# Optimization experiments

Measured on AMD Instinct MI355X. Metric: run time of the kernel, lower is better.

## Reference

```python
import jax, jax.numpy as jnp
import numpy as np

D_IN, D_OUT, K = 128, 256, 16
B, N = 2, 16384
D_HALF = D_OUT // 2
EPS = 1e-6
GROUPS = 16


def conv1x1(x, w, b):
    # x: (B,C,N,K), w: (O,C), b: (O,)
    return jnp.einsum('oc,bcnk->bonk', w, x) + b[None, :, None, None]


def groupnorm(x, w, b, groups=GROUPS):
    Bv, C, Nv, Kv = x.shape
    xr = x.reshape(Bv, groups, C // groups, Nv, Kv)
    m = xr.mean(axis=(2, 3, 4), keepdims=True)
    v = xr.var(axis=(2, 3, 4), keepdims=True)
    xn = ((xr - m) / jnp.sqrt(v + EPS)).reshape(Bv, C, Nv, Kv)
    return xn * w[None, :, None, None] + b[None, :, None, None]


def lse(coords, x, idx, dist, w, b, gw, gb):
    # coords: (B,N,3); x: (B,C,N,1); idx: (B,N,K); dist: (B,N,K)
    nbr = jax.vmap(lambda c, i: c[i])(coords, idx)          # (B,N,K,3)
    ctr = jnp.broadcast_to(coords[:, :, None, :], nbr.shape)  # (B,N,K,3)
    rel = jnp.concatenate([ctr, nbr, ctr - nbr], axis=-1)    # (B,N,K,9)
    geo = jnp.concatenate([rel.transpose(0, 3, 1, 2), dist[:, None, :, :]], axis=1)  # (B,10,N,K)
    geo = jax.nn.relu(groupnorm(conv1x1(geo, w, b), gw, gb))  # (B,d/2,N,K)
    nf = jax.vmap(lambda f, i: f[:, i])(x[..., 0], idx)       # (B,d/2,N,K)
    return jnp.concatenate([geo, nf], axis=1)                 # (B,d,N,K)


def attentive_pool(x, w, b, gw, gb):
    m = x.mean(axis=-1, keepdims=True)  # (B,C,N,1)
    return jax.nn.relu(groupnorm(conv1x1(m, w, b), gw, gb))


def setup_inputs() -> dict:
    key = jax.random.key(0)
    ks = jax.random.split(key, 16)
    s = 0.02
    d = {
        'coords': jax.random.normal(ks[0], (B, N, 3), jnp.float32),
        'features': jax.random.normal(ks[1], (B, D_IN, N, 1), jnp.float32),
        'knn_dist': jax.random.uniform(ks[2], (B, N, K), jnp.float32),
        'knn_idx': jax.random.randint(ks[3], (B, N, K), 0, N),
        'w1': jax.random.normal(ks[4], (D_HALF, D_IN), jnp.float32) * s,
        'b1': jnp.zeros((D_HALF,), jnp.float32),
        'lse1_w': jax.random.normal(ks[5], (D_HALF, 10), jnp.float32) * s,
        'lse1_b': jnp.zeros((D_HALF,), jnp.float32),
        'lse1_gw': jnp.ones((D_HALF,), jnp.float32),
        'lse1_gb': jnp.zeros((D_HALF,), jnp.float32),
        'pool1_w': jax.random.normal(ks[6], (D_HALF, D_OUT), jnp.float32) * s,
        'pool1_b': jnp.zeros((D_HALF,), jnp.float32),
        'pool1_gw': jnp.ones((D_HALF,), jnp.float32),
        'pool1_gb': jnp.zeros((D_HALF,), jnp.float32),
        'lse2_w': jax.random.normal(ks[7], (D_HALF, 10), jnp.float32) * s,
        'lse2_b': jnp.zeros((D_HALF,), jnp.float32),
        'lse2_gw': jnp.ones((D_HALF,), jnp.float32),
        'lse2_gb': jnp.zeros((D_HALF,), jnp.float32),
        'pool2_w': jax.random.normal(ks[8], (D_OUT, D_OUT), jnp.float32) * s,
        'pool2_b': jnp.zeros((D_OUT,), jnp.float32),
        'pool2_gw': jnp.ones((D_OUT,), jnp.float32),
        'pool2_gb': jnp.zeros((D_OUT,), jnp.float32),
        'mlp2_w': jax.random.normal(ks[9], (2 * D_OUT, D_OUT), jnp.float32) * s,
        'mlp2_b': jnp.zeros((2 * D_OUT,), jnp.float32),
        'sc_w': jax.random.normal(ks[10], (2 * D_OUT, D_IN), jnp.float32) * s,
        'sc_b': jnp.zeros((2 * D_OUT,), jnp.float32),
        'sc_gw': jnp.ones((2 * D_OUT,), jnp.float32),
        'sc_gb': jnp.zeros((2 * D_OUT,), jnp.float32),
    }
    return d


def reference(coords, features, knn_dist, knn_idx,
              w1, b1,
              lse1_w, lse1_b, lse1_gw, lse1_gb,
              pool1_w, pool1_b, pool1_gw, pool1_gb,
              lse2_w, lse2_b, lse2_gw, lse2_gb,
              pool2_w, pool2_b, pool2_gw, pool2_gb,
              mlp2_w, mlp2_b, sc_w, sc_b, sc_gw, sc_gb):
    # mlp1: conv + LeakyReLU(0.2), no norm
    x = jax.nn.leaky_relu(conv1x1(features, w1, b1), 0.2)        # (B,d/2,N,1)
    x = lse(coords, x, knn_idx, knn_dist, lse1_w, lse1_b, lse1_gw, lse1_gb)  # (B,d,N,K)
    x = attentive_pool(x, pool1_w, pool1_b, pool1_gw, pool1_gb)  # (B,d/2,N,1)
    x = lse(coords, x, knn_idx, knn_dist, lse2_w, lse2_b, lse2_gw, lse2_gb)  # (B,d,N,K)
    x = attentive_pool(x, pool2_w, pool2_b, pool2_gw, pool2_gb)  # (B,d,N,1)
    main = conv1x1(x, mlp2_w, mlp2_b)                            # (B,2d,N,1)
    short = groupnorm(conv1x1(features, sc_w, sc_b), sc_gw, sc_gb)
    return jax.nn.leaky_relu(main + short, 0.01)                 # (B,2d,N,1)
```

## Files before the change

kernel.cpp:

```cpp
#include <hip/hip_runtime.h>


constexpr int Bc = 2;
constexpr int Nc = 16384;
constexpr int Kc = 16;
constexpr float EPSc = 1e-6f;

typedef __attribute__((ext_vector_type(8))) short short8;
typedef __attribute__((ext_vector_type(4))) short short4v;
typedef __attribute__((ext_vector_type(4))) float floatx4;

__device__ inline short f2bf(float x) {
    union { float f; unsigned u; } v; v.f = x;
    unsigned r = v.u + 0x7fffu + ((v.u >> 16) & 1u);
    return (short)(r >> 16);
}
__device__ inline float bf2f(short s) {
    union { unsigned u; float f; } v;
    v.u = ((unsigned)(unsigned short)s) << 16;
    return v.f;
}

constexpr size_t OW_P1W = 0;
constexpr size_t OW_P2W = OW_P1W + 128*256;
constexpr size_t OW_M2W = OW_P2W + 256*256;
constexpr size_t OW_SCW = OW_M2W + 512*256;
constexpr size_t OW_W1  = OW_SCW + 512*128;
constexpr size_t OW_L1W = OW_W1  + 128*128;
constexpr size_t OW_L2W = OW_L1W + 128*32;
constexpr size_t OW_FB  = OW_L2W + 128*32;
constexpr size_t OW_X1  = OW_FB  + (size_t)Bc*Nc*128;
constexpr size_t OW_M   = OW_X1  + (size_t)Bc*Nc*128;
constexpr size_t OW_Z1  = OW_M   + (size_t)Bc*Nc*256;
constexpr size_t OW_Z2  = OW_Z1  + (size_t)Bc*Nc*128;
constexpr size_t OW_S   = OW_Z2  + (size_t)Bc*Nc*256;

constexpr int CV0 = 128*256;
constexpr int CV1 = CV0 + 256*256;
constexpr int CV2 = CV1 + 512*256;
constexpr int CV3 = CV2 + 512*128;
constexpr int CV4 = CV3 + 128*128;
constexpr int CV5 = CV4 + 128*32;
constexpr int CV6 = CV5 + 128*32;
constexpr int CVTOT = CV6 + 512;

__global__ void prep_kernel(const float* __restrict__ p1w,
                            const float* __restrict__ p2w,
                            const float* __restrict__ m2w,
                            const float* __restrict__ scw,
                            const float* __restrict__ w1,
                            const float* __restrict__ l1w,
                            const float* __restrict__ l2w,
                            short* __restrict__ W16,
                            float* __restrict__ ST)
{
    int i = blockIdx.x * 256 + threadIdx.x;
    if (i < CV0) { W16[OW_P1W + i] = f2bf(p1w[i]); return; }
    if (i < CV1) { int k = i - CV0; W16[OW_P2W + k] = f2bf(p2w[k]); return; }
    if (i < CV2) { int k = i - CV1; W16[OW_M2W + k] = f2bf(m2w[k]); return; }
    if (i < CV3) { int k = i - CV2; W16[OW_SCW + k] = f2bf(scw[k]); return; }
    if (i < CV4) { int k = i - CV3; W16[OW_W1  + k] = f2bf(w1[k]); return; }
    if (i < CV5) { int k = i - CV4; int o = k >> 5, c = k & 31;
                   W16[OW_L1W + k] = (c < 10) ? f2bf(l1w[o*10+c]) : (short)0; return; }
    if (i < CV6) { int k = i - CV5; int o = k >> 5, c = k & 31;
                   W16[OW_L2W + k] = (c < 10) ? f2bf(l2w[o*10+c]) : (short)0; return; }
    { int k = i - CV6; if (k < 512) ST[k] = 0.f; }
}

__global__ void feat_t_kernel(const float* __restrict__ in, short* __restrict__ out) {
    int tid  = threadIdx.x;
    int lane = tid & 63, wave = tid >> 6;
    int bb = blockIdx.x / (Nc / 64);
    int n  = (blockIdx.x % (Nc / 64)) * 64 + lane;
    #pragma unroll
    for (int cc = 0; cc < 4; cc++) {
        int c0 = (wave + cc * 4) * 8;
        short8 sv;
        #pragma unroll
        for (int i = 0; i < 8; i++)
            sv[i] = f2bf(in[((size_t)bb * 128 + c0 + i) * Nc + n]);
        *(short8*)&out[((size_t)(bb * Nc + n)) * 128 + c0] = sv;
    }
}

__launch_bounds__(256)
__global__ void geo_reduce_kernel(const float* __restrict__ coords,
                                  const int* __restrict__ knn_idx,
                                  const float* __restrict__ knn_dist,
                                  float* __restrict__ dst)
{
    __shared__ float part[4][65];
    const int tid  = threadIdx.x;
    const int b    = blockIdx.y;
    const int base = blockIdx.x * 256 + tid;
    const float* cb  = coords   + (size_t)b * Nc * 3;
    const int*   ib  = knn_idx  + (size_t)b * Nc * Kc;
    const float* db  = knn_dist + (size_t)b * Nc * Kc;

    float acc[65];
    #pragma unroll
    for (int i = 0; i < 65; i++) acc[i] = 0.f;

    #pragma unroll
    for (int it = 0; it < 4; it++) {
        int r = base + it * 65536;
        int n = r >> 4;
        float cx = cb[n*3+0], cy = cb[n*3+1], cz = cb[n*3+2];
        int   j  = ib[r];
        float nx = cb[j*3+0], ny = cb[j*3+1], nz = cb[j*3+2];
        float d  = db[r];
        float g[10] = {cx,cy,cz,nx,ny,nz,cx-nx,cy-ny,cz-nz,d};
        #pragma unroll
        for (int c = 0; c < 10; c++) acc[c] += g[c];
        int idx = 10;
        #pragma unroll
        for (int c = 0; c < 10; c++)
            #pragma unroll
            for (int c2 = c; c2 < 10; c2++) acc[idx++] += g[c] * g[c2];
    }
    #pragma unroll
    for (int i = 0; i < 65; i++) {
        float v = acc[i];
        #pragma unroll
        for (int off = 1; off < 64; off <<= 1) v += __shfl_xor(v, off);
        acc[i] = v;
    }
    int lane = tid & 63, wave = tid >> 6;
    if (lane == 0) {
        #pragma unroll
        for (int i = 0; i < 65; i++) part[wave][i] = acc[i];
    }
    __syncthreads();
    if (tid < 65) {
        float s = part[0][tid] + part[1][tid] + part[2][tid] + part[3][tid];
        atomicAdd(&dst[b * 65 + tid], s);
    }
}

__launch_bounds__(512)
__global__ void lse_param_kernel(const float* __restrict__ geoS,
                                 const float* __restrict__ l1w,
                                 const float* __restrict__ l1b,
                                 const float* __restrict__ l1gw,
                                 const float* __restrict__ l1gb,
                                 const float* __restrict__ l2w,
                                 const float* __restrict__ l2b,
                                 const float* __restrict__ l2gw,
                                 const float* __restrict__ l2gb,
                                 float* __restrict__ lp)
{
    __shared__ float osum[512], osq[512];
    const int tid = threadIdx.x;
    const int s = tid >> 8, r = tid & 255, b = r >> 7, o = r & 127;
    const float* wf = s ? l2w : l1w;
    const float* bf = s ? l2b : l1b;
    const float* gwf = s ? l2gw : l1gw;
    const float* gbf = s ? l2gb : l1gb;
    const float NK = (float)(Nc * Kc);
    const float* S = geoS + b * 65;

    float w[10];
    #pragma unroll
    for (int c = 0; c < 10; c++) w[c] = wf[o * 10 + c];
    float wS = 0.f;
    #pragma unroll
    for (int c = 0; c < 10; c++) wS += w[c] * S[c];
    float q = 0.f;
    {
        int idx = 10;
        #pragma unroll
        for (int c = 0; c < 10; c++)
            #pragma unroll
            for (int c2 = c; c2 < 10; c2++) {
                float t = w[c] * w[c2] * S[idx++];
                q += (c == c2) ? t : 2.f * t;
            }
    }
    float bo = bf[o];
    osum[tid] = NK * bo + wS;
    osq[tid]  = NK * bo * bo + 2.f * bo * wS + q;
    __syncthreads();
    int gb0 = tid & ~7;
    float gs = 0.f, gq = 0.f;
    #pragma unroll
    for (int i = 0; i < 8; i++) { gs += osum[gb0 + i]; gq += osq[gb0 + i]; }
    float cnt  = 8.f * NK;
    float mean = gs / cnt;
    float var  = gq / cnt - mean * mean;
    float iv   = rsqrtf(var + EPSc);
    float psc  = iv * gwf[o];
    float psh  = (bo - mean) * psc + gbf[o];
    lp[s * 512 + b * 256 + o]       = psc;
    lp[s * 512 + b * 256 + 128 + o] = psh;
}

template<int CIN, int COUT, int GROUP_CH, int MODE>
__launch_bounds__(256)
__global__ void gemm_conv(const short* __restrict__ wA,
                          const short* __restrict__ xB,
                          const float* __restrict__ bias,
                          short* __restrict__ outb,
                          float* __restrict__ outf,
                          float* __restrict__ stats,
                          const short* __restrict__ sbuf,
                          const float* __restrict__ st_sc,
                          const float* __restrict__ gw,
                          const float* __restrict__ gb,
                          float sc_cnt,
                          const float* __restrict__ bst,
                          const float* __restrict__ bgw,
                          const float* __restrict__ bgb,
                          float bcnt,
                          const float* __restrict__ bias2,
                          short* __restrict__ outb2)
{
    __shared__ short Abuf[128 * 40];
    __shared__ short Bbuf[128 * 40];
    __shared__ float sstat[32];
    __shared__ float smean[4], sinv[4];
    __shared__ float bsc[256], bsh[256];

    const int tid  = threadIdx.x;
    const int n0   = blockIdx.x * 128;
    const int mo   = blockIdx.y * 128;
    const int b    = blockIdx.z;
    const int lane = tid & 63;
    const int wave = tid >> 6;
    const int wm   = (wave >> 1) * 64;
    const int wn   = (wave & 1) * 64;
    const int l15  = lane & 15;
    const int quad = lane >> 4;
    const bool sc_tile = (MODE == 4) && (mo < 512);

    if constexpr (MODE == 2 || MODE == 4) { if (tid < 32) sstat[tid] = 0.f; }
    if constexpr (MODE == 3) {
        if (tid < 4) {
            int g = (mo >> 5) + tid;
            float s0 = st_sc[(b * 16 + g) * 2 + 0];
            float s1 = st_sc[(b * 16 + g) * 2 + 1];
            float mean = s0 / sc_cnt;
            float var  = s1 / sc_cnt - mean * mean;
            smean[tid] = mean;
            sinv[tid]  = rsqrtf(var + EPSc);
        }
        if (tid < CIN) {
            int g = tid >> 4;
            float s0 = bst[(b * 16 + g) * 2 + 0];
            float s1 = bst[(b * 16 + g) * 2 + 1];
            float mean = s0 / bcnt;
            float var  = s1 / bcnt - mean * mean;
            float inv  = rsqrtf(var + EPSc);
            float sc_  = inv * bgw[tid];
            bsc[tid] = sc_;
            bsh[tid] = bgb[tid] - mean * sc_;
        }
    }

    floatx4 acc[4][4];
    #pragma unroll
    for (int mi = 0; mi < 4; mi++)
        #pragma unroll
        for (int ni = 0; ni < 4; ni++)
            acc[mi][ni] = (floatx4){0.f, 0.f, 0.f, 0.f};

    const short* wAr = wA + (size_t)mo * CIN;
    const short* xBr = xB + (size_t)b * Nc * CIN + (size_t)n0 * CIN;

    for (int c0 = 0; c0 < CIN; c0 += 32) {
        __syncthreads();
        #pragma unroll
        for (int s = 0; s < 2; s++) {
            int e = tid + s * 256;
            int r = e >> 2, q = e & 3;
            *(short8*)&Abuf[r * 40 + q * 8] =
                *(const short8*)(wAr + (size_t)r * CIN + c0 + q * 8);
            short8 v = *(const short8*)(xBr + (size_t)r * CIN + c0 + q * 8);
            if constexpr (MODE == 3) {
                #pragma unroll
                for (int i = 0; i < 8; i++) {
                    int ch = c0 + q * 8 + i;
                    float t = bf2f(v[i]) * bsc[ch] + bsh[ch];
                    v[i] = f2bf(t > 0.f ? t : 0.f);
                }
            }
            *(short8*)&Bbuf[r * 40 + q * 8] = v;
        }
        __syncthreads();

        short8 af[4], bfr[4];
        #pragma unroll
        for (int mi = 0; mi < 4; mi++)
            af[mi] = *(short8*)&Abuf[(wm + mi * 16 + l15) * 40 + quad * 8];
        #pragma unroll
        for (int ni = 0; ni < 4; ni++)
            bfr[ni] = *(short8*)&Bbuf[(wn + ni * 16 + l15) * 40 + quad * 8];
        #pragma unroll
        for (int mi = 0; mi < 4; mi++)
            #pragma unroll
            for (int ni = 0; ni < 4; ni++)
                acc[mi][ni] = __builtin_amdgcn_mfma_f32_16x16x32_bf16(
                    af[mi], bfr[ni], acc[mi][ni], 0, 0, 0);
    }

    #pragma unroll
    for (int mi = 0; mi < 4; mi++) {
        int rowl = wm + mi * 16 + quad * 4;
        float b4[4], gw4[4], gb4[4];
        #pragma unroll
        for (int r = 0; r < 4; r++) {
            if constexpr (MODE == 4) {
                b4[r] = sc_tile ? bias[mo + rowl + r] : bias2[mo - 512 + rowl + r];
            } else {
                b4[r] = bias[mo + rowl + r];
            }
            if constexpr (MODE == 3) {
                gw4[r] = gw[mo + rowl + r];
                gb4[r] = gb[mo + rowl + r];
            }
        }
        float gs = 0.f, gq = 0.f;
        #pragma unroll
        for (int ni = 0; ni < 4; ni++) {
            int col = n0 + wn + ni * 16 + l15;
            if constexpr (MODE == 3) {
                short4v s4 = *(const short4v*)&sbuf[((size_t)(b * Nc + col)) * 512 + mo + rowl];
                int gl = rowl >> 5;
                #pragma unroll
                for (int r = 0; r < 4; r++) {
                    float v = acc[mi][ni][r] + b4[r];
                    float s = bf2f(s4[r]);
                    float sn = (s - smean[gl]) * sinv[gl] * gw4[r] + gb4[r];
                    float o = v + sn;
                    o = o > 0.f ? o : 0.01f * o;
                    outf[((size_t)b * COUT + mo + rowl + r) * Nc + col] = o;
                }
            } else if constexpr (MODE == 4) {
                short4v sv;
                #pragma unroll
                for (int r = 0; r < 4; r++) {
                    float v = acc[mi][ni][r] + b4[r];
                    if (sc_tile) { gs += v; gq += v * v; }
                    else v = v > 0.f ? v : 0.2f * v;
                    sv[r] = f2bf(v);
                }
                if (sc_tile)
                    *(short4v*)&outb[((size_t)(b * Nc + col)) * 512 + mo + rowl] = sv;
                else
                    *(short4v*)&outb2[((size_t)(b * Nc + col)) * 128 + mo - 512 + rowl] = sv;
            } else {
                short4v sv;
                #pragma unroll
                for (int r = 0; r < 4; r++) {
                    float v = acc[mi][ni][r] + b4[r];
                    if constexpr (MODE == 1) v = v > 0.f ? v : 0.2f * v;
                    if constexpr (MODE == 2) { gs += v; gq += v * v; }
                    sv[r] = f2bf(v);
                }
                *(short4v*)&outb[((size_t)(b * Nc + col)) * COUT + mo + rowl] = sv;
            }
        }
        if ((MODE == 2) || (MODE == 4 && sc_tile)) {
            #pragma unroll
            for (int off = 1; off < 16; off <<= 1) {
                gs += __shfl_xor(gs, off);
                gq += __shfl_xor(gq, off);
            }
            if (l15 == 0) {
                int gl = rowl / GROUP_CH;
                atomicAdd(&sstat[gl * 2 + 0], gs);
                atomicAdd(&sstat[gl * 2 + 1], gq);
            }
        }
    }
    if ((MODE == 2) || (MODE == 4 && sc_tile)) {
        __syncthreads();
        constexpr int NG = 128 / GROUP_CH;
        if (tid < 2 * NG) {
            int g0 = mo / GROUP_CH;
            atomicAdd(&stats[b * 32 + (g0 + (tid >> 1)) * 2 + (tid & 1)], sstat[tid]);
        }
    }
}

__launch_bounds__(256)
__global__ void lse_m_kernel(const float* __restrict__ coords,
                             const int* __restrict__ knn_idx,
                             const float* __restrict__ knn_dist,
                             const short* __restrict__ xprev,
                             const short* __restrict__ wpad,
                             const float* __restrict__ lp,
                             const float* __restrict__ xst,
                             const float* __restrict__ xgw,
                             const float* __restrict__ xgb,
                             float xcnt,
                             short* __restrict__ m)
{
    __shared__ short Bbuf[256 * 40];
    __shared__ int   jl[256];
    __shared__ float xscs[128], xshs[128];

    const int tid = threadIdx.x;
    const int b   = blockIdx.x >> 10;
    const int n0  = (blockIdx.x & 1023) * 16;
    const bool norm = (xst != nullptr);

    if (norm && tid < 128) {
        int g = tid >> 3;
        float s0 = xst[(b * 16 + g) * 2 + 0];
        float s1 = xst[(b * 16 + g) * 2 + 1];
        float mean = s0 / xcnt;
        float var  = s1 / xcnt - mean * mean;
        float inv  = rsqrtf(var + EPSc);
        float sc_  = inv * xgw[tid];
        xscs[tid] = sc_;
        xshs[tid] = xgb[tid] - mean * sc_;
    }
    {
        int pt = tid & 15, k = tid >> 4;
        int n  = n0 + pt;
        const float* cb = coords + (size_t)b * Nc * 3;
        float cx = cb[n*3+0], cy = cb[n*3+1], cz = cb[n*3+2];
        int   j  = knn_idx[((size_t)b * Nc + n) * Kc + k];
        float nx = cb[j*3+0], ny = cb[j*3+1], nz = cb[j*3+2];
        float d  = knn_dist[((size_t)b * Nc + n) * Kc + k];
        int col = k * 16 + pt;
        short8 w0, w1, zz;
        w0[0]=f2bf(cx); w0[1]=f2bf(cy); w0[2]=f2bf(cz);
        w0[3]=f2bf(nx); w0[4]=f2bf(ny); w0[5]=f2bf(nz);
        w0[6]=f2bf(cx-nx); w0[7]=f2bf(cy-ny);
        w1[0]=f2bf(cz-nz); w1[1]=f2bf(d);
        #pragma unroll
        for (int i = 2; i < 8; i++) w1[i] = 0;
        #pragma unroll
        for (int i = 0; i < 8; i++) zz[i] = 0;
        *(short8*)&Bbuf[col * 40 + 0]  = w0;
        *(short8*)&Bbuf[col * 40 + 8]  = w1;
        *(short8*)&Bbuf[col * 40 + 16] = zz;
        *(short8*)&Bbuf[col * 40 + 24] = zz;
        jl[col] = j;
    }
    __syncthreads();

    const int lane = tid & 63, wave = tid >> 6;
    const int l15 = lane & 15, quad = lane >> 4;
    short8 bfr[16];
    #pragma unroll
    for (int ni = 0; ni < 16; ni++)
        bfr[ni] = *(short8*)&Bbuf[(ni * 16 + l15) * 40 + quad * 8];
    #pragma unroll
    for (int mt2 = 0; mt2 < 2; mt2++) {
        int mt = wave * 2 + mt2;
        short8 af = *(const short8*)(wpad + (mt * 16 + l15) * 32 + quad * 8);
        floatx4 acc[16];
        #pragma unroll
        for (int ni = 0; ni < 16; ni++) {
            acc[ni] = (floatx4){0.f, 0.f, 0.f, 0.f};
            acc[ni] = __builtin_amdgcn_mfma_f32_16x16x32_bf16(af, bfr[ni], acc[ni], 0, 0, 0);
        }
        short4v sv;
        #pragma unroll
        for (int r = 0; r < 4; r++) {
            int o = mt * 16 + quad * 4 + r;
            float psc = lp[b * 256 + o];
            float psh = lp[b * 256 + 128 + o];
            float s = 0.f;
            #pragma unroll
            for (int ni = 0; ni < 16; ni++) {
                float v = acc[ni][r] * psc + psh;
                s += v > 0.f ? v : 0.f;
            }
            sv[r] = f2bf(s * (1.f / 16.f));
        }
        *(short4v*)&m[((size_t)(b * Nc + n0 + l15)) * 256 + mt * 16 + quad * 4] = sv;
    }

    {
        int tp = tid & 15, cs = tid >> 4;
        float sc8[8], sh8[8];
        if (norm) {
            #pragma unroll
            for (int i = 0; i < 8; i++) { sc8[i] = xscs[cs*8+i]; sh8[i] = xshs[cs*8+i]; }
        }
        float acc8[8];
        #pragma unroll
        for (int i = 0; i < 8; i++) acc8[i] = 0.f;
        #pragma unroll
        for (int k = 0; k < 16; k++) {
            int j = jl[k * 16 + tp];
            short8 v = *(const short8*)&xprev[((size_t)(b * Nc + j)) * 128 + cs * 8];
            if (norm) {
                #pragma unroll
                for (int i = 0; i < 8; i++) {
                    float t = bf2f(v[i]) * sc8[i] + sh8[i];
                    acc8[i] += t > 0.f ? t : 0.f;
                }
            } else {
                #pragma unroll
                for (int i = 0; i < 8; i++) acc8[i] += bf2f(v[i]);
            }
        }
        short8 sv;
        #pragma unroll
        for (int i = 0; i < 8; i++) sv[i] = f2bf(acc8[i] * (1.f / 16.f));
        *(short8*)&m[((size_t)(b * Nc + n0 + tp)) * 256 + 128 + cs * 8] = sv;
    }
}

extern "C" void kernel_launch(void* const* d_in, const int* in_sizes, int n_in,
                              void* d_out, int out_size, void* d_ws, size_t ws_size,
                              hipStream_t stream)
{
    const float* coords   = (const float*)d_in[0];
    const float* features = (const float*)d_in[1];
    const float* knn_dist = (const float*)d_in[2];
    const int*   knn_idx  = (const int*)  d_in[3];
    const float* w1       = (const float*)d_in[4];
    const float* b1       = (const float*)d_in[5];
    const float* lse1_w   = (const float*)d_in[6];
    const float* lse1_b   = (const float*)d_in[7];
    const float* lse1_gw  = (const float*)d_in[8];
    const float* lse1_gb  = (const float*)d_in[9];
    const float* pool1_w  = (const float*)d_in[10];
    const float* pool1_b  = (const float*)d_in[11];
    const float* pool1_gw = (const float*)d_in[12];
    const float* pool1_gb = (const float*)d_in[13];
    const float* lse2_w   = (const float*)d_in[14];
    const float* lse2_b   = (const float*)d_in[15];
    const float* lse2_gw  = (const float*)d_in[16];
    const float* lse2_gb  = (const float*)d_in[17];
    const float* pool2_w  = (const float*)d_in[18];
    const float* pool2_b  = (const float*)d_in[19];
    const float* pool2_gw = (const float*)d_in[20];
    const float* pool2_gb = (const float*)d_in[21];
    const float* mlp2_w   = (const float*)d_in[22];
    const float* mlp2_b   = (const float*)d_in[23];
    const float* sc_w     = (const float*)d_in[24];
    const float* sc_b     = (const float*)d_in[25];
    const float* sc_gw    = (const float*)d_in[26];
    const float* sc_gb    = (const float*)d_in[27];
    (void)in_sizes; (void)n_in; (void)out_size; (void)ws_size;

    float* ST = (float*)d_ws;
    float* ST_SC  = ST + 0;
    float* ST_P1  = ST + 64;
    float* ST_P2  = ST + 128;
    float* ST_GEO = ST + 256;
    float* ST_LP  = ST + 512;
    short* W16 = (short*)(ST + 2048);
    short* P1Wb = W16 + OW_P1W;
    short* P2Wb = W16 + OW_P2W;
    short* M2Wb = W16 + OW_M2W;
    short* SCWb = W16 + OW_SCW;
    short* L1Wb = W16 + OW_L1W;
    short* L2Wb = W16 + OW_L2W;
    short* FB   = W16 + OW_FB;
    short* X1B  = W16 + OW_X1;
    short* MB   = W16 + OW_M;
    short* Z1   = W16 + OW_Z1;
    short* Z2   = W16 + OW_Z2;
    short* SB   = W16 + OW_S;
    float* out  = (float*)d_out;

    prep_kernel<<<(CVTOT + 255) / 256, 256, 0, stream>>>(
        pool1_w, pool2_w, mlp2_w, sc_w, w1, lse1_w, lse2_w, W16, ST);
    feat_t_kernel<<<Bc * Nc / 64, 256, 0, stream>>>(features, FB);
    geo_reduce_kernel<<<dim3(256, Bc), 256, 0, stream>>>(
        coords, knn_idx, knn_dist, ST_GEO);
    lse_param_kernel<<<1, 512, 0, stream>>>(
        ST_GEO, lse1_w, lse1_b, lse1_gw, lse1_gb,
        lse2_w, lse2_b, lse2_gw, lse2_gb, ST_LP);

    gemm_conv<128,640,32,4><<<dim3(Nc/128, 5, Bc), 256, 0, stream>>>(
        SCWb, FB, sc_b, SB, nullptr, ST_SC, nullptr, nullptr, nullptr, nullptr, 0.f,
        nullptr, nullptr, nullptr, 0.f, b1, X1B);
    lse_m_kernel<<<Bc * Nc / 16, 256, 0, stream>>>(
        coords, knn_idx, knn_dist, X1B, L1Wb, ST_LP,
        nullptr, nullptr, nullptr, 0.f, MB);
    gemm_conv<256,128,8,2><<<dim3(Nc/128, 1, Bc), 256, 0, stream>>>(
        P1Wb, MB, pool1_b, Z1, nullptr, ST_P1, nullptr, nullptr, nullptr, nullptr, 0.f,
        nullptr, nullptr, nullptr, 0.f, nullptr, nullptr);
    lse_m_kernel<<<Bc * Nc / 16, 256, 0, stream>>>(
        coords, knn_idx, knn_dist, Z1, L2Wb, ST_LP + 512,
        ST_P1, pool1_gw, pool1_gb, (float)(8 * Nc), MB);
    gemm_conv<256,256,16,2><<<dim3(Nc/128, 2, Bc), 256, 0, stream>>>(
        P2Wb, MB, pool2_b, Z2, nullptr, ST_P2, nullptr, nullptr, nullptr, nullptr, 0.f,
        nullptr, nullptr, nullptr, 0.f, nullptr, nullptr);
    gemm_conv<256,512,32,3><<<dim3(Nc/128, 4, Bc), 256, 0, stream>>>(
        M2Wb, Z2, mlp2_b, nullptr, out, nullptr, SB, ST_SC, sc_gw, sc_gb,
        (float)(32 * Nc), ST_P2, pool2_gw, pool2_gb, (float)(16 * Nc),
        nullptr, nullptr);
}
```

Before: 334.7 us.

## Restructure LSE kernel to per-wave point tiles without shared memory

Rewrites the local spatial encoding kernel so each wave owns 16 points. The geometric B-operand is built directly in registers (quad-specialised) instead of staging through LDS, and the neighbour indices are loaded once as int4 vectors and reused for both the geometry MFMA and the feature gather. The grid shrinks from 2048 to 512 blocks, with an XCD-aware block-to-tile mapping. GroupNorm scale and shift for the second pass move into a separate tiny kernel, and NORM becomes a template parameter. The aim is to remove LDS traffic and barriers and to improve locality, at the cost of more register pressure, an extra launch and fewer blocks in flight.

```diff
diff --git a/kernel.cpp b/kernel.cpp
--- a/kernel.cpp
+++ b/kernel.cpp
@@ -9,6 +9,7 @@
 typedef __attribute__((ext_vector_type(8))) short short8;
 typedef __attribute__((ext_vector_type(4))) short short4v;
 typedef __attribute__((ext_vector_type(4))) float floatx4;
+typedef __attribute__((ext_vector_type(4))) int intx4;
 
 __device__ inline short f2bf(float x) {
     union { float f; unsigned u; } v; v.f = x;
@@ -192,6 +193,26 @@
     float psh  = (bo - mean) * psc + gbf[o];
     lp[s * 512 + b * 256 + o]       = psc;
     lp[s * 512 + b * 256 + 128 + o] = psh;
+}
+
+__global__ void pool_param_kernel(const float* __restrict__ st,
+                                  const float* __restrict__ gw,
+                                  const float* __restrict__ gb,
+                                  float cnt,
+                                  float* __restrict__ osc,
+                                  float* __restrict__ osh)
+{
+    int tid = threadIdx.x;
+    int b = tid >> 7, c = tid & 127;
+    int g = c >> 3;
+    float s0 = st[(b * 16 + g) * 2 + 0];
+    float s1 = st[(b * 16 + g) * 2 + 1];
+    float mean = s0 / cnt;
+    float var  = s1 / cnt - mean * mean;
+    float inv  = rsqrtf(var + EPSc);
+    float sc = inv * gw[c];
+    osc[b * 128 + c] = sc;
+    osh[b * 128 + c] = gb[c] - mean * sc;
 }
 
 template<int CIN, int COUT, int GROUP_CH, int MODE>
@@ -382,6 +403,7 @@
     }
 }
 
+template<bool NORM>
 __launch_bounds__(256)
 __global__ void lse_m_kernel(const float* __restrict__ coords,
                              const int* __restrict__ knn_idx,
@@ -389,120 +411,143 @@
                              const short* __restrict__ xprev,
                              const short* __restrict__ wpad,
                              const float* __restrict__ lp,
-                             const float* __restrict__ xst,
-                             const float* __restrict__ xgw,
-                             const float* __restrict__ xgb,
-                             float xcnt,
+                             const float* __restrict__ xscg,
+                             const float* __restrict__ xshg,
                              short* __restrict__ m)
 {
-    __shared__ short Bbuf[256 * 40];
-    __shared__ int   jl[256];
-    __shared__ float xscs[128], xshs[128];
-
-    const int tid = threadIdx.x;
-    const int b   = blockIdx.x >> 10;
-    const int n0  = (blockIdx.x & 1023) * 16;
-    const bool norm = (xst != nullptr);
-
-    if (norm && tid < 128) {
-        int g = tid >> 3;
-        float s0 = xst[(b * 16 + g) * 2 + 0];
-        float s1 = xst[(b * 16 + g) * 2 + 1];
-        float mean = s0 / xcnt;
-        float var  = s1 / xcnt - mean * mean;
-        float inv  = rsqrtf(var + EPSc);
-        float sc_  = inv * xgw[tid];
-        xscs[tid] = sc_;
-        xshs[tid] = xgb[tid] - mean * sc_;
-    }
-    {
-        int pt = tid & 15, k = tid >> 4;
-        int n  = n0 + pt;
-        const float* cb = coords + (size_t)b * Nc * 3;
-        float cx = cb[n*3+0], cy = cb[n*3+1], cz = cb[n*3+2];
-        int   j  = knn_idx[((size_t)b * Nc + n) * Kc + k];
-        float nx = cb[j*3+0], ny = cb[j*3+1], nz = cb[j*3+2];
-        float d  = knn_dist[((size_t)b * Nc + n) * Kc + k];
-        int col = k * 16 + pt;
-        short8 w0, w1, zz;
-        w0[0]=f2bf(cx); w0[1]=f2bf(cy); w0[2]=f2bf(cz);
-        w0[3]=f2bf(nx); w0[4]=f2bf(ny); w0[5]=f2bf(nz);
-        w0[6]=f2bf(cx-nx); w0[7]=f2bf(cy-ny);
-        w1[0]=f2bf(cz-nz); w1[1]=f2bf(d);
-        #pragma unroll
-        for (int i = 2; i < 8; i++) w1[i] = 0;
-        #pragma unroll
-        for (int i = 0; i < 8; i++) zz[i] = 0;
-        *(short8*)&Bbuf[col * 40 + 0]  = w0;
-        *(short8*)&Bbuf[col * 40 + 8]  = w1;
-        *(short8*)&Bbuf[col * 40 + 16] = zz;
-        *(short8*)&Bbuf[col * 40 + 24] = zz;
-        jl[col] = j;
-    }
-    __syncthreads();
-
-    const int lane = tid & 63, wave = tid >> 6;
-    const int l15 = lane & 15, quad = lane >> 4;
-    short8 bfr[16];
-    #pragma unroll
-    for (int ni = 0; ni < 16; ni++)
-        bfr[ni] = *(short8*)&Bbuf[(ni * 16 + l15) * 40 + quad * 8];
-    #pragma unroll
-    for (int mt2 = 0; mt2 < 2; mt2++) {
-        int mt = wave * 2 + mt2;
-        short8 af = *(const short8*)(wpad + (mt * 16 + l15) * 32 + quad * 8);
-        floatx4 acc[16];
-        #pragma unroll
-        for (int ni = 0; ni < 16; ni++) {
-            acc[ni] = (floatx4){0.f, 0.f, 0.f, 0.f};
-            acc[ni] = __builtin_amdgcn_mfma_f32_16x16x32_bf16(af, bfr[ni], acc[ni], 0, 0, 0);
-        }
+    const int tid  = threadIdx.x;
+    const int wave = tid >> 6, lane = tid & 63;
+    const int l15  = lane & 15, quad = lane >> 4;
+    const int xcd  = blockIdx.x & 7;
+    const int b    = xcd >> 2;
+    const int tile = (blockIdx.x >> 3) * 16 + (xcd & 3) * 4 + wave;
+    const int n    = tile * 16 + l15;
+
+    const int* irow = knn_idx + ((size_t)(b * Nc) + n) * Kc;
+    int jn[16];
+    #pragma unroll
+    for (int i = 0; i < 4; i++) {
+        intx4 t = *(const intx4*)(irow + i * 4);
+        jn[i*4+0] = t.x; jn[i*4+1] = t.y; jn[i*4+2] = t.z; jn[i*4+3] = t.w;
+    }
+    const float* cb = coords + (size_t)b * Nc * 3;
+
+    floatx4 osum[8];
+    #pragma unroll
+    for (int mt = 0; mt < 8; mt++) osum[mt] = (floatx4){0.f, 0.f, 0.f, 0.f};
+
+    #pragma unroll
+    for (int h = 0; h < 2; h++) {
+        short8 bfr[8];
+        if (quad == 0) {
+            float cx = cb[n*3+0], cy = cb[n*3+1], cz = cb[n*3+2];
+            #pragma unroll
+            for (int i = 0; i < 8; i++) {
+                int j = jn[h*8+i];
+                float nx = cb[j*3+0], ny = cb[j*3+1], nz = cb[j*3+2];
+                short8 t;
+                t[0]=f2bf(cx); t[1]=f2bf(cy); t[2]=f2bf(cz);
+                t[3]=f2bf(nx); t[4]=f2bf(ny); t[5]=f2bf(nz);
+                t[6]=f2bf(cx-nx); t[7]=f2bf(cy-ny);
+                bfr[i] = t;
+            }
+        } else if (quad == 1) {
+            float cz = cb[n*3+2];
+            const float* drow = knn_dist + ((size_t)(b * Nc) + n) * Kc;
+            floatx4 d0 = *(const floatx4*)(drow + h*8);
+            floatx4 d1 = *(const floatx4*)(drow + h*8 + 4);
+            #pragma unroll
+            for (int i = 0; i < 8; i++) {
+                int j = jn[h*8+i];
+                float nz = cb[j*3+2];
+                float dd = (i < 4) ? d0[i & 3] : d1[i & 3];
+                short8 t;
+                t[0] = f2bf(cz - nz); t[1] = f2bf(dd);
+                #pragma unroll
+                for (int q = 2; q < 8; q++) t[q] = 0;
+                bfr[i] = t;
+            }
+        } else {
+            #pragma unroll
+            for (int i = 0; i < 8; i++) {
+                short8 t;
+                #pragma unroll
+                for (int q = 0; q < 8; q++) t[q] = 0;
+                bfr[i] = t;
+            }
+        }
+        #pragma unroll
+        for (int mt = 0; mt < 8; mt++) {
+            short8 af = *(const short8*)(wpad + (mt * 16 + l15) * 32 + quad * 8);
+            floatx4 acc[8];
+            #pragma unroll
+            for (int i = 0; i < 8; i++)
+                acc[i] = __builtin_amdgcn_mfma_f32_16x16x32_bf16(
+                    af, bfr[i], (floatx4){0.f,0.f,0.f,0.f}, 0, 0, 0);
+            floatx4 psc = *(const floatx4*)&lp[b * 256 + mt * 16 + quad * 4];
+            floatx4 psh = *(const floatx4*)&lp[b * 256 + 128 + mt * 16 + quad * 4];
+            #pragma unroll
+            for (int r = 0; r < 4; r++) {
+                float s = 0.f;
+                #pragma unroll
+                for (int i = 0; i < 8; i++) {
+                    float v = acc[i][r] * psc[r] + psh[r];
+                    s += v > 0.f ? v : 0.f;
+                }
+                osum[mt][r] += s;
+            }
+        }
+    }
+    #pragma unroll
+    for (int mt = 0; mt < 8; mt++) {
         short4v sv;
         #pragma unroll
-        for (int r = 0; r < 4; r++) {
-            int o = mt * 16 + quad * 4 + r;
-            float psc = lp[b * 256 + o];
-            float psh = lp[b * 256 + 128 + o];
-            float s = 0.f;
-            #pragma unroll
-            for (int ni = 0; ni < 16; ni++) {
-                float v = acc[ni][r] * psc + psh;
-                s += v > 0.f ? v : 0.f;
-            }
-            sv[r] = f2bf(s * (1.f / 16.f));
-        }
-        *(short4v*)&m[((size_t)(b * Nc + n0 + l15)) * 256 + mt * 16 + quad * 4] = sv;
-    }
-
-    {
-        int tp = tid & 15, cs = tid >> 4;
-        float sc8[8], sh8[8];
-        if (norm) {
-            #pragma unroll
-            for (int i = 0; i < 8; i++) { sc8[i] = xscs[cs*8+i]; sh8[i] = xshs[cs*8+i]; }
-        }
-        float acc8[8];
-        #pragma unroll
-        for (int i = 0; i < 8; i++) acc8[i] = 0.f;
+        for (int r = 0; r < 4; r++) sv[r] = f2bf(osum[mt][r] * (1.f / 16.f));
+        *(short4v*)&m[((size_t)(b * Nc + n)) * 256 + mt * 16 + quad * 4] = sv;
+    }
+
+    const short* xb = xprev + ((size_t)(b * Nc)) * 128;
+    #pragma unroll
+    for (int ch = 0; ch < 2; ch++) {
+        int c0 = quad * 32 + ch * 16;
+        float sc16[16], sh16[16];
+        if (NORM) {
+            #pragma unroll
+            for (int i = 0; i < 4; i++) {
+                floatx4 a = *(const floatx4*)&xscg[b * 128 + c0 + i * 4];
+                floatx4 s = *(const floatx4*)&xshg[b * 128 + c0 + i * 4];
+                #pragma unroll
+                for (int r = 0; r < 4; r++) { sc16[i*4+r] = a[r]; sh16[i*4+r] = s[r]; }
+            }
+        }
+        float ga[16];
+        #pragma unroll
+        for (int i = 0; i < 16; i++) ga[i] = 0.f;
         #pragma unroll
         for (int k = 0; k < 16; k++) {
-            int j = jl[k * 16 + tp];
-            short8 v = *(const short8*)&xprev[((size_t)(b * Nc + j)) * 128 + cs * 8];
-            if (norm) {
-                #pragma unroll
-                for (int i = 0; i < 8; i++) {
-                    float t = bf2f(v[i]) * sc8[i] + sh8[i];
-                    acc8[i] += t > 0.f ? t : 0.f;
+            const short* row = xb + (size_t)jn[k] * 128 + c0;
+            short8 v0 = *(const short8*)row;
+            short8 v1 = *(const short8*)(row + 8);
+            #pragma unroll
+            for (int i = 0; i < 8; i++) {
+                float t0 = bf2f(v0[i]);
+                float t1 = bf2f(v1[i]);
+                if (NORM) {
+                    t0 = t0 * sc16[i] + sh16[i];     t0 = t0 > 0.f ? t0 : 0.f;
+                    t1 = t1 * sc16[8+i] + sh16[8+i]; t1 = t1 > 0.f ? t1 : 0.f;
                 }
-            } else {
-                #pragma unroll
-                for (int i = 0; i < 8; i++) acc8[i] += bf2f(v[i]);
-            }
-        }
-        short8 sv;
-        #pragma unroll
-        for (int i = 0; i < 8; i++) sv[i] = f2bf(acc8[i] * (1.f / 16.f));
-        *(short8*)&m[((size_t)(b * Nc + n0 + tp)) * 256 + 128 + cs * 8] = sv;
+                ga[i] += t0; ga[8+i] += t1;
+            }
+        }
+        short8 s0, s1;
+        #pragma unroll
+        for (int i = 0; i < 8; i++) {
+            s0[i] = f2bf(ga[i] * (1.f / 16.f));
+            s1[i] = f2bf(ga[8+i] * (1.f / 16.f));
+        }
+        short* mp = &m[((size_t)(b * Nc + n)) * 256 + 128 + c0];
+        *(short8*)mp = s0;
+        *(short8*)(mp + 8) = s1;
     }
 }
 
@@ -546,6 +591,8 @@
     float* ST_P2  = ST + 128;
     float* ST_GEO = ST + 256;
     float* ST_LP  = ST + 512;
+    float* ST_XSC = ST + 1536;
+    float* ST_XSH = ST + 1792;
     short* W16 = (short*)(ST + 2048);
     short* P1Wb = W16 + OW_P1W;
     short* P2Wb = W16 + OW_P2W;
@@ -573,15 +620,15 @@
     gemm_conv<128,640,32,4><<<dim3(Nc/128, 5, Bc), 256, 0, stream>>>(
         SCWb, FB, sc_b, SB, nullptr, ST_SC, nullptr, nullptr, nullptr, nullptr, 0.f,
         nullptr, nullptr, nullptr, 0.f, b1, X1B);
-    lse_m_kernel<<<Bc * Nc / 16, 256, 0, stream>>>(
-        coords, knn_idx, knn_dist, X1B, L1Wb, ST_LP,
-        nullptr, nullptr, nullptr, 0.f, MB);
+    lse_m_kernel<false><<<512, 256, 0, stream>>>(
+        coords, knn_idx, knn_dist, X1B, L1Wb, ST_LP, nullptr, nullptr, MB);
     gemm_conv<256,128,8,2><<<dim3(Nc/128, 1, Bc), 256, 0, stream>>>(
         P1Wb, MB, pool1_b, Z1, nullptr, ST_P1, nullptr, nullptr, nullptr, nullptr, 0.f,
         nullptr, nullptr, nullptr, 0.f, nullptr, nullptr);
-    lse_m_kernel<<<Bc * Nc / 16, 256, 0, stream>>>(
-        coords, knn_idx, knn_dist, Z1, L2Wb, ST_LP + 512,
-        ST_P1, pool1_gw, pool1_gb, (float)(8 * Nc), MB);
+    pool_param_kernel<<<1, 256, 0, stream>>>(
+        ST_P1, pool1_gw, pool1_gb, (float)(8 * Nc), ST_XSC, ST_XSH);
+    lse_m_kernel<true><<<512, 256, 0, stream>>>(
+        coords, knn_idx, knn_dist, Z1, L2Wb, ST_LP + 512, ST_XSC, ST_XSH, MB);
     gemm_conv<256,256,16,2><<<dim3(Nc/128, 2, Bc), 256, 0, stream>>>(
         P2Wb, MB, pool2_b, Z2, nullptr, ST_P2, nullptr, nullptr, nullptr, nullptr, 0.f,
         nullptr, nullptr, nullptr, 0.f, nullptr, nullptr);
```

Result: slower. 360.7 us (+7.8%).
